# Kernel tuning notes

Measured on AMD Instinct MI355X. Metric: run time of the kernel, lower is better.

Reference implementation:

```python
import jax, jax.numpy as jnp
import numpy as np

B, F, O = 32, 26, 20
IN, G = 2048, 512
REL = 53
EPS = 1e-5  # BatchNorm1d default eps


def setup_inputs() -> dict:
    key = jax.random.key(0)
    ks = jax.random.split(key, 10)
    inp = {
        "region_feats": jax.random.normal(ks[0], (B, F, O, IN), jnp.float32),
        "region_masks": jnp.ones((B, F, O), jnp.float32),
        "rel_feats": jax.random.randint(ks[1], (B, F, O, O), 0, REL, jnp.int64),
        "tem_feats": jax.random.uniform(ks[2], (B, F * O, F * O), jnp.float32),
        # learned params (eval mode: dropout off, BN uses running stats)
        "rel_W": jax.random.normal(ks[3], (G, IN), jnp.float32) * (1.0 / np.sqrt(IN)),
        "rel_b": jnp.zeros((G,), jnp.float32),
        "rel_emb": jax.random.normal(ks[4], (REL, G), jnp.float32) * 0.02,
        "tem_W": jax.random.normal(ks[5], (G, IN), jnp.float32) * (1.0 / np.sqrt(IN)),
        "tem_b": jnp.zeros((G,), jnp.float32),
        "bn_w": jnp.ones((F * O,), jnp.float32),
        "bn_b": jnp.zeros((F * O,), jnp.float32),
        "bn_rm": jnp.zeros((F * O,), jnp.float32),
        "bn_rv": jnp.ones((F * O,), jnp.float32),
    }
    return inp


def reference(region_feats, region_masks, rel_feats, tem_feats,
              rel_W, rel_b, rel_emb, tem_W, tem_b,
              bn_w, bn_b, bn_rm, bn_rv):
    b, f, o, _ = region_feats.shape
    # ---- RELATIONAL FEATURE GRAPH ----
    # [B,F,O,G]
    rel_region = jnp.einsum("bfoi,gi->bfog", region_feats, rel_W) + rel_b
    # embedding lookup: [B,F,O,O,G]
    emb = rel_emb[rel_feats]
    mask = (rel_feats > 0).astype(region_feats.dtype)  # [B,F,O,O]
    msum = jnp.sum(mask, axis=3)                        # [B,F,O]
    # sum_j mask_ij * emb_ij  (masked reduction over neighbor dim)
    emb_sum = jnp.einsum("bfijg,bfij->bfig", emb, mask)
    # sum_j mask_ij * r_i == r_i * msum_i, so (emb_sum + r*msum)/msum
    rel_out = (emb_sum + rel_region * msum[..., None]) / msum[..., None]
    rel_out = rel_out.reshape(b, f * o, -1)
    # ---- TEMPORAL FEATURE GRAPH ----
    tem_region = jnp.einsum("bfoi,gi->bfog", region_feats, tem_W) + tem_b
    tem_region = tem_region.reshape(b, f * o, -1)
    tem_sum = jnp.sum(tem_feats, axis=2)                # [B, F*O]
    tem_out = jnp.matmul(tem_feats, tem_region) / tem_sum[..., None]
    # ---- OUTPUT ----
    out = jnp.concatenate([rel_out, tem_out], axis=-1)  # [B, F*O, 2G]
    out = jnp.tanh(out)
    # BatchNorm1d over channel dim 1 (eval mode, running stats)
    inv = bn_w / jnp.sqrt(bn_rv + EPS)                  # [F*O]
    out = (out - bn_rm[None, :, None]) * inv[None, :, None] + bn_b[None, :, None]
    return out
```

## Files before the change

### kernel.cpp

```cpp
#include <hip/hip_runtime.h>
#include <stdint.h>

#define BB 32
#define FO 520
#define M1 16640
#define KIN 2048
#define KA 2112
#define N1 1024
#define GG 512
#define K2 544
#define M2 640

typedef unsigned short u16;
typedef short v8s __attribute__((ext_vector_type(8)));
typedef float v4f __attribute__((ext_vector_type(4)));

__device__ __forceinline__ u16 f2bf(float f) {
  union { float f; unsigned u; } v; v.f = f;
  unsigned r = v.u + 0x7fffu + ((v.u >> 16) & 1u);
  return (u16)(r >> 16);
}

__device__ __forceinline__ float fast_tanh(float x) {
  float cx = fminf(fmaxf(x, -15.f), 15.f);
  float e = __expf(2.f * cx);
  return (e - 1.f) / (e + 1.f);
}

__global__ void cast8_kernel(const float* __restrict__ rf, const int* __restrict__ rel,
                             u16* __restrict__ A1) {
  const int m = blockIdx.x;
  const int t = threadIdx.x;
  const float4* p = (const float4*)(rf + (size_t)m * KIN);
  u16* orow = A1 + (size_t)m * KA;
  float4 a = p[2 * t], b = p[2 * t + 1];
  v8s v;
  v[0] = (short)f2bf(a.x); v[1] = (short)f2bf(a.y);
  v[2] = (short)f2bf(a.z); v[3] = (short)f2bf(a.w);
  v[4] = (short)f2bf(b.x); v[5] = (short)f2bf(b.y);
  v[6] = (short)f2bf(b.z); v[7] = (short)f2bf(b.w);
  *(v8s*)(orow + t * 8) = v;
  if (t < 64) {
    const int* rp = rel + (size_t)m * 20;
    int cnt = 0, ms = 0;
#pragma unroll
    for (int j = 0; j < 20; ++j) {
      int ix = rp[j];
      cnt += (ix == t + 1);
      ms += (ix > 0);
    }
    float sval = (t < 52 && ms > 0) ? (float)cnt / (float)ms : 0.f;
    orow[KIN + t] = f2bf(sval);
  }
}

__global__ void castw_kernel(const float* __restrict__ relW, const float* __restrict__ temW,
                             const float* __restrict__ emb, u16* __restrict__ o) {
  const int n = blockIdx.x;
  u16* orow = o + (size_t)n * KA;
  const float* src = (n < GG) ? (relW + (size_t)n * KIN) : (temW + (size_t)(n - GG) * KIN);
  for (int k = threadIdx.x; k < KIN; k += 256) orow[k] = f2bf(src[k]);
  for (int k = KIN + threadIdx.x; k < KA; k += 256) {
    int l = k - KIN;
    float v = (n < GG && l < 52) ? emb[(size_t)(l + 1) * GG + n] : 0.f;
    orow[k] = f2bf(v);
  }
}

__global__ void casta2_kernel(const float* __restrict__ tem, u16* __restrict__ A2,
                              float* __restrict__ tsum) {
  const int w = threadIdx.x >> 6;
  const int l = threadIdx.x & 63;
  const int row = blockIdx.x * 4 + w;
  const int b = row / M2, i = row % M2;
  u16* orow = A2 + (size_t)row * K2;
  v8s z = {0, 0, 0, 0, 0, 0, 0, 0};
  if (i >= FO) {
    *(v8s*)(orow + l * 8) = z;
    if (l < 4) *(v8s*)(orow + (64 + l) * 8) = z;
    return;
  }
  const float* srow = tem + ((size_t)b * FO + i) * FO;
  float s = 0.f;
#pragma unroll
  for (int pass = 0; pass < 2; ++pass) {
    int c = (pass == 0) ? l : (64 + l);
    if (pass == 1 && l >= 4) break;
    if (c < 65) {
      float4 a = *(const float4*)(srow + 8 * c);
      float4 bb = *(const float4*)(srow + 8 * c + 4);
      s += a.x + a.y + a.z + a.w + bb.x + bb.y + bb.z + bb.w;
      v8s v;
      v[0] = (short)f2bf(a.x); v[1] = (short)f2bf(a.y);
      v[2] = (short)f2bf(a.z); v[3] = (short)f2bf(a.w);
      v[4] = (short)f2bf(bb.x); v[5] = (short)f2bf(bb.y);
      v[6] = (short)f2bf(bb.z); v[7] = (short)f2bf(bb.w);
      *(v8s*)(orow + c * 8) = v;
    } else {
      *(v8s*)(orow + c * 8) = z;
    }
  }
#pragma unroll
  for (int off = 32; off > 0; off >>= 1) s += __shfl_down(s, off);
  if (l == 0) tsum[(size_t)b * FO + i] = s;
}

__global__ void transp_kernel(const u16* __restrict__ in, u16* __restrict__ o) {
  __shared__ u16 tile[64][66];
  const int jb = blockIdx.x;
  const int gb = blockIdx.y;
  const int b = blockIdx.z;
  const int tx = threadIdx.x, ty = threadIdx.y;
#pragma unroll
  for (int r = 0; r < 8; ++r) {
    int jl = ty + 8 * r;
    int j = jb * 64 + jl;
    unsigned v = 0;
    if (j < FO) v = *(const unsigned*)(in + ((size_t)b * FO + j) * GG + gb * 64 + 2 * tx);
    tile[2 * tx][jl] = (u16)(v & 0xffff);
    tile[2 * tx + 1][jl] = (u16)(v >> 16);
  }
  __syncthreads();
#pragma unroll
  for (int r = 0; r < 8; ++r) {
    int gl = ty + 8 * r;
    int j2 = jb * 64 + 2 * tx;
    if (j2 < K2) {
      unsigned v = *(const unsigned*)&tile[gl][2 * tx];
      *(unsigned*)(o + ((size_t)b * GG + gb * 64 + gl) * K2 + j2) = v;
    }
  }
}

__global__ __launch_bounds__(256) void gemm1_kernel(
    const u16* __restrict__ A, const u16* __restrict__ Wc,
    const float* __restrict__ rel_b, const float* __restrict__ tem_b,
    const float* __restrict__ bn_w, const float* __restrict__ bn_b,
    const float* __restrict__ bn_rm, const float* __restrict__ bn_rv,
    float* __restrict__ out, u16* __restrict__ tem_nat) {
  __shared__ u16 As[128 * 32];
  __shared__ u16 Bs[128 * 32];
  const int tid = threadIdx.x;
  const int lane = tid & 63;
  const int wv = tid >> 6, wm = wv >> 1, wn = wv & 1;
  const int id = blockIdx.x;
  const int x = id & 7, s = id >> 3;
  int mt, ntile;
  if (s < 128) { mt = x * 16 + (s >> 3); ntile = s & 7; }
  else         { mt = 128 + (s - 128);   ntile = x; }
  const int m0 = mt * 128;
  const int n0 = ntile * 128;
  const int quad = lane >> 4, r16 = lane & 15;

  v4f acc[4][4];
#pragma unroll
  for (int i = 0; i < 4; ++i)
#pragma unroll
    for (int j = 0; j < 4; ++j) { v4f z = {0.f, 0.f, 0.f, 0.f}; acc[i][j] = z; }

  for (int k0 = 0; k0 < KA; k0 += 32) {
    __syncthreads();
#pragma unroll
    for (int i = 0; i < 2; ++i) {
      const int L = i * 256 + tid;
      const int r = L >> 2, c = L & 3;
      const u16* ga = A + (size_t)(m0 + r) * KA + k0 + c * 8;
      const u16* gb = Wc + (size_t)(n0 + r) * KA + k0 + c * 8;
      u16* la = &As[(size_t)(i * 256 + wv * 64) * 8];
      u16* lb = &Bs[(size_t)(i * 256 + wv * 64) * 8];
      __builtin_amdgcn_global_load_lds((const __attribute__((address_space(1))) void*)ga,
                                       (__attribute__((address_space(3))) void*)la, 16, 0, 0);
      __builtin_amdgcn_global_load_lds((const __attribute__((address_space(1))) void*)gb,
                                       (__attribute__((address_space(3))) void*)lb, 16, 0, 0);
    }
    __syncthreads();
    v8s af[4], bf[4];
#pragma unroll
    for (int t = 0; t < 4; ++t) {
      af[t] = *(const v8s*)&As[(wm * 64 + t * 16 + r16) * 32 + quad * 8];
      bf[t] = *(const v8s*)&Bs[(wn * 64 + t * 16 + r16) * 32 + quad * 8];
    }
#pragma unroll
    for (int mtt = 0; mtt < 4; ++mtt)
#pragma unroll
      for (int ntt = 0; ntt < 4; ++ntt)
        acc[mtt][ntt] = __builtin_amdgcn_mfma_f32_16x16x32_bf16(af[mtt], bf[ntt], acc[mtt][ntt], 0, 0, 0);
  }

  const bool relhalf = (n0 < GG);
#pragma unroll
  for (int mtt = 0; mtt < 4; ++mtt) {
#pragma unroll
    for (int ntt = 0; ntt < 4; ++ntt) {
      const int n = n0 + wn * 64 + ntt * 16 + r16;
      const int mbase = m0 + wm * 64 + mtt * 16 + quad * 4;
#pragma unroll
      for (int r = 0; r < 4; ++r) {
        const int m = mbase + r;
        float v = acc[mtt][ntt][r];
        if (relhalf) {
          v += rel_b[n];
          const int fo = m % FO;
          float inv = bn_w[fo] * rsqrtf(bn_rv[fo] + 1e-5f);
          out[(size_t)m * N1 + n] = (fast_tanh(v) - bn_rm[fo]) * inv + bn_b[fo];
        } else {
          v += tem_b[n - GG];
          tem_nat[(size_t)m * GG + (n - GG)] = f2bf(v);
        }
      }
    }
  }
}

__global__ __launch_bounds__(256) void gemm2_kernel(
    const u16* __restrict__ A2, const u16* __restrict__ BT,
    const float* __restrict__ tsum,
    const float* __restrict__ bn_w, const float* __restrict__ bn_b,
    const float* __restrict__ bn_rm, const float* __restrict__ bn_rv,
    float* __restrict__ out) {
  __shared__ u16 As[128 * 32];
  __shared__ u16 Bs[128 * 32];
  const int tid = threadIdx.x;
  const int lane = tid & 63;
  const int wv = tid >> 6, wm = wv >> 1, wn = wv & 1;
  const int m0 = blockIdx.x * 128;
  const int n0 = blockIdx.y * 128;
  const int b = blockIdx.z;
  const u16* Ab = A2 + (size_t)b * M2 * K2;
  const u16* Bb = BT + (size_t)b * GG * K2;
  const int quad = lane >> 4, r16 = lane & 15;

  v4f acc[4][4];
#pragma unroll
  for (int i = 0; i < 4; ++i)
#pragma unroll
    for (int j = 0; j < 4; ++j) { v4f z = {0.f, 0.f, 0.f, 0.f}; acc[i][j] = z; }

  for (int k0 = 0; k0 < K2; k0 += 32) {
    __syncthreads();
#pragma unroll
    for (int i = 0; i < 2; ++i) {
      const int L = i * 256 + tid;
      const int r = L >> 2, c = L & 3;
      const u16* ga = Ab + (size_t)(m0 + r) * K2 + k0 + c * 8;
      const u16* gb = Bb + (size_t)(n0 + r) * K2 + k0 + c * 8;
      u16* la = &As[(size_t)(i * 256 + wv * 64) * 8];
      u16* lb = &Bs[(size_t)(i * 256 + wv * 64) * 8];
      __builtin_amdgcn_global_load_lds((const __attribute__((address_space(1))) void*)ga,
                                       (__attribute__((address_space(3))) void*)la, 16, 0, 0);
      __builtin_amdgcn_global_load_lds((const __attribute__((address_space(1))) void*)gb,
                                       (__attribute__((address_space(3))) void*)lb, 16, 0, 0);
    }
    __syncthreads();
    v8s af[4], bf[4];
#pragma unroll
    for (int t = 0; t < 4; ++t) {
      af[t] = *(const v8s*)&As[(wm * 64 + t * 16 + r16) * 32 + quad * 8];
      bf[t] = *(const v8s*)&Bs[(wn * 64 + t * 16 + r16) * 32 + quad * 8];
    }
#pragma unroll
    for (int mt = 0; mt < 4; ++mt)
#pragma unroll
      for (int nt = 0; nt < 4; ++nt)
        acc[mt][nt] = __builtin_amdgcn_mfma_f32_16x16x32_bf16(af[mt], bf[nt], acc[mt][nt], 0, 0, 0);
  }

#pragma unroll
  for (int mt = 0; mt < 4; ++mt) {
#pragma unroll
    for (int nt = 0; nt < 4; ++nt) {
      const int g = n0 + wn * 64 + nt * 16 + r16;
      const int ibase = m0 + wm * 64 + mt * 16 + quad * 4;
#pragma unroll
      for (int r = 0; r < 4; ++r) {
        const int i = ibase + r;
        if (i < FO) {
          float v = acc[mt][nt][r] / tsum[(size_t)b * FO + i];
          float inv = bn_w[i] * rsqrtf(bn_rv[i] + 1e-5f);
          out[((size_t)(b * FO + i)) * N1 + GG + g] =
              (fast_tanh(v) - bn_rm[i]) * inv + bn_b[i];
        }
      }
    }
  }
}

extern "C" void kernel_launch(void* const* d_in, const int* in_sizes, int n_in,
                              void* d_out, int out_size, void* d_ws, size_t ws_size,
                              hipStream_t stream) {
  const float* region_feats = (const float*)d_in[0];
  const int* rel_feats = (const int*)d_in[2];
  const float* tem_feats = (const float*)d_in[3];
  const float* rel_W = (const float*)d_in[4];
  const float* rel_b = (const float*)d_in[5];
  const float* rel_emb = (const float*)d_in[6];
  const float* tem_W = (const float*)d_in[7];
  const float* tem_b = (const float*)d_in[8];
  const float* bn_w = (const float*)d_in[9];
  const float* bn_b = (const float*)d_in[10];
  const float* bn_rm = (const float*)d_in[11];
  const float* bn_rv = (const float*)d_in[12];
  float* out = (float*)d_out;

  char* base = (char*)d_ws;
  u16* A1 = (u16*)base;
  u16* BT = (u16*)base;
  u16* Wc = (u16*)(base + 70287360);
  u16* A2 = (u16*)(base + 74612736);
  u16* tem_nat = (u16*)(base + 96894976);
  float* tsum = (float*)(base + 113934336);

  cast8_kernel<<<16640, 256, 0, stream>>>(region_feats, rel_feats, A1);
  castw_kernel<<<1024, 256, 0, stream>>>(rel_W, tem_W, rel_emb, Wc);
  casta2_kernel<<<5120, 256, 0, stream>>>(tem_feats, A2, tsum);
  gemm1_kernel<<<1040, 256, 0, stream>>>(A1, Wc, rel_b, tem_b,
                                         bn_w, bn_b, bn_rm, bn_rv, out, tem_nat);
  transp_kernel<<<dim3(9, 8, 32), dim3(32, 8), 0, stream>>>(tem_nat, BT);
  gemm2_kernel<<<dim3(5, 4, 32), 256, 0, stream>>>(A2, BT, tsum,
                                                   bn_w, bn_b, bn_rm, bn_rv, out);
}
```

Measured before the change: 461.8 us.

## Fuse weight cast and transpose into neighbours, use BK=64 with XOR-swizzled LDS

Result: faster. 451.5 us (-2.2%).

```diff
diff --git a/kernel.cpp b/kernel.cpp
--- a/kernel.cpp
+++ b/kernel.cpp
@@ -8,7 +8,7 @@
 #define KA 2112
 #define N1 1024
 #define GG 512
-#define K2 544
+#define K2P 576
 #define M2 640
 
 typedef unsigned short u16;
@@ -27,12 +27,23 @@
   return (e - 1.f) / (e + 1.f);
 }
 
-__global__ void cast8_kernel(const float* __restrict__ rf, const int* __restrict__ rel,
-                             u16* __restrict__ A1) {
-  const int m = blockIdx.x;
+__global__ void prep_kernel(const float* __restrict__ rf, const int* __restrict__ rel,
+                            const float* __restrict__ relW, const float* __restrict__ temW,
+                            const float* __restrict__ emb,
+                            u16* __restrict__ A1, u16* __restrict__ Wc) {
+  const int blk = blockIdx.x;
   const int t = threadIdx.x;
-  const float4* p = (const float4*)(rf + (size_t)m * KIN);
-  u16* orow = A1 + (size_t)m * KA;
+  const float* src;
+  u16* orow;
+  if (blk < M1) {
+    src = rf + (size_t)blk * KIN;
+    orow = A1 + (size_t)blk * KA;
+  } else {
+    const int n = blk - M1;
+    src = (n < GG) ? (relW + (size_t)n * KIN) : (temW + (size_t)(n - GG) * KIN);
+    orow = Wc + (size_t)n * KA;
+  }
+  const float4* p = (const float4*)src;
   float4 a = p[2 * t], b = p[2 * t + 1];
   v8s v;
   v[0] = (short)f2bf(a.x); v[1] = (short)f2bf(a.y);
@@ -41,29 +52,22 @@
   v[6] = (short)f2bf(b.z); v[7] = (short)f2bf(b.w);
   *(v8s*)(orow + t * 8) = v;
   if (t < 64) {
-    const int* rp = rel + (size_t)m * 20;
-    int cnt = 0, ms = 0;
-#pragma unroll
-    for (int j = 0; j < 20; ++j) {
-      int ix = rp[j];
-      cnt += (ix == t + 1);
-      ms += (ix > 0);
-    }
-    float sval = (t < 52 && ms > 0) ? (float)cnt / (float)ms : 0.f;
+    float sval = 0.f;
+    if (blk < M1) {
+      const int* rp = rel + (size_t)blk * 20;
+      int cnt = 0, ms = 0;
+#pragma unroll
+      for (int j = 0; j < 20; ++j) {
+        int ix = rp[j];
+        cnt += (ix == t + 1);
+        ms += (ix > 0);
+      }
+      if (t < 52 && ms > 0) sval = (float)cnt / (float)ms;
+    } else {
+      const int n = blk - M1;
+      if (n < GG && t < 52) sval = emb[(size_t)(t + 1) * GG + n];
+    }
     orow[KIN + t] = f2bf(sval);
-  }
-}
-
-__global__ void castw_kernel(const float* __restrict__ relW, const float* __restrict__ temW,
-                             const float* __restrict__ emb, u16* __restrict__ o) {
-  const int n = blockIdx.x;
-  u16* orow = o + (size_t)n * KA;
-  const float* src = (n < GG) ? (relW + (size_t)n * KIN) : (temW + (size_t)(n - GG) * KIN);
-  for (int k = threadIdx.x; k < KIN; k += 256) orow[k] = f2bf(src[k]);
-  for (int k = KIN + threadIdx.x; k < KA; k += 256) {
-    int l = k - KIN;
-    float v = (n < GG && l < 52) ? emb[(size_t)(l + 1) * GG + n] : 0.f;
-    orow[k] = f2bf(v);
   }
 }
 
@@ -73,63 +77,44 @@
   const int l = threadIdx.x & 63;
   const int row = blockIdx.x * 4 + w;
   const int b = row / M2, i = row % M2;
-  u16* orow = A2 + (size_t)row * K2;
+  u16* orow = A2 + (size_t)row * K2P;
   v8s z = {0, 0, 0, 0, 0, 0, 0, 0};
   if (i >= FO) {
     *(v8s*)(orow + l * 8) = z;
-    if (l < 4) *(v8s*)(orow + (64 + l) * 8) = z;
+    if (l < 8) *(v8s*)(orow + (64 + l) * 8) = z;
     return;
   }
   const float* srow = tem + ((size_t)b * FO + i) * FO;
   float s = 0.f;
-#pragma unroll
-  for (int pass = 0; pass < 2; ++pass) {
-    int c = (pass == 0) ? l : (64 + l);
-    if (pass == 1 && l >= 4) break;
-    if (c < 65) {
-      float4 a = *(const float4*)(srow + 8 * c);
-      float4 bb = *(const float4*)(srow + 8 * c + 4);
+  {
+    float4 a = *(const float4*)(srow + 8 * l);
+    float4 bb = *(const float4*)(srow + 8 * l + 4);
+    s += a.x + a.y + a.z + a.w + bb.x + bb.y + bb.z + bb.w;
+    v8s v;
+    v[0] = (short)f2bf(a.x); v[1] = (short)f2bf(a.y);
+    v[2] = (short)f2bf(a.z); v[3] = (short)f2bf(a.w);
+    v[4] = (short)f2bf(bb.x); v[5] = (short)f2bf(bb.y);
+    v[6] = (short)f2bf(bb.z); v[7] = (short)f2bf(bb.w);
+    *(v8s*)(orow + l * 8) = v;
+  }
+  if (l < 8) {
+    if (l == 0) {
+      float4 a = *(const float4*)(srow + 512);
+      float4 bb = *(const float4*)(srow + 516);
       s += a.x + a.y + a.z + a.w + bb.x + bb.y + bb.z + bb.w;
       v8s v;
       v[0] = (short)f2bf(a.x); v[1] = (short)f2bf(a.y);
       v[2] = (short)f2bf(a.z); v[3] = (short)f2bf(a.w);
       v[4] = (short)f2bf(bb.x); v[5] = (short)f2bf(bb.y);
       v[6] = (short)f2bf(bb.z); v[7] = (short)f2bf(bb.w);
-      *(v8s*)(orow + c * 8) = v;
+      *(v8s*)(orow + 512) = v;
     } else {
-      *(v8s*)(orow + c * 8) = z;
+      *(v8s*)(orow + (64 + l) * 8) = z;
     }
   }
 #pragma unroll
   for (int off = 32; off > 0; off >>= 1) s += __shfl_down(s, off);
   if (l == 0) tsum[(size_t)b * FO + i] = s;
-}
-
-__global__ void transp_kernel(const u16* __restrict__ in, u16* __restrict__ o) {
-  __shared__ u16 tile[64][66];
-  const int jb = blockIdx.x;
-  const int gb = blockIdx.y;
-  const int b = blockIdx.z;
-  const int tx = threadIdx.x, ty = threadIdx.y;
-#pragma unroll
-  for (int r = 0; r < 8; ++r) {
-    int jl = ty + 8 * r;
-    int j = jb * 64 + jl;
-    unsigned v = 0;
-    if (j < FO) v = *(const unsigned*)(in + ((size_t)b * FO + j) * GG + gb * 64 + 2 * tx);
-    tile[2 * tx][jl] = (u16)(v & 0xffff);
-    tile[2 * tx + 1][jl] = (u16)(v >> 16);
-  }
-  __syncthreads();
-#pragma unroll
-  for (int r = 0; r < 8; ++r) {
-    int gl = ty + 8 * r;
-    int j2 = jb * 64 + 2 * tx;
-    if (j2 < K2) {
-      unsigned v = *(const unsigned*)&tile[gl][2 * tx];
-      *(unsigned*)(o + ((size_t)b * GG + gb * 64 + gl) * K2 + j2) = v;
-    }
-  }
 }
 
 __global__ __launch_bounds__(256) void gemm1_kernel(
@@ -137,9 +122,10 @@
     const float* __restrict__ rel_b, const float* __restrict__ tem_b,
     const float* __restrict__ bn_w, const float* __restrict__ bn_b,
     const float* __restrict__ bn_rm, const float* __restrict__ bn_rv,
-    float* __restrict__ out, u16* __restrict__ tem_nat) {
-  __shared__ u16 As[128 * 32];
-  __shared__ u16 Bs[128 * 32];
+    float* __restrict__ out, u16* __restrict__ BT) {
+  __shared__ u16 smem[128 * 132];
+  u16* As = smem;
+  u16* Bs = smem + 128 * 64;
   const int tid = threadIdx.x;
   const int lane = tid & 63;
   const int wv = tid >> 6, wm = wv >> 1, wn = wv & 1;
@@ -148,8 +134,7 @@
   int mt, ntile;
   if (s < 128) { mt = x * 16 + (s >> 3); ntile = s & 7; }
   else         { mt = 128 + (s - 128);   ntile = x; }
-  const int m0 = mt * 128;
-  const int n0 = ntile * 128;
+  const int m0 = mt * 128, n0 = ntile * 128;
   const int quad = lane >> 4, r16 = lane & 15;
 
   v4f acc[4][4];
@@ -158,12 +143,13 @@
 #pragma unroll
     for (int j = 0; j < 4; ++j) { v4f z = {0.f, 0.f, 0.f, 0.f}; acc[i][j] = z; }
 
-  for (int k0 = 0; k0 < KA; k0 += 32) {
-    __syncthreads();
-#pragma unroll
-    for (int i = 0; i < 2; ++i) {
+  for (int k0 = 0; k0 < KA; k0 += 64) {
+    __syncthreads();
+#pragma unroll
+    for (int i = 0; i < 4; ++i) {
       const int L = i * 256 + tid;
-      const int r = L >> 2, c = L & 3;
+      const int r = L >> 3;
+      const int c = (L & 7) ^ (r & 7);
       const u16* ga = A + (size_t)(m0 + r) * KA + k0 + c * 8;
       const u16* gb = Wc + (size_t)(n0 + r) * KA + k0 + c * 8;
       u16* la = &As[(size_t)(i * 256 + wv * 64) * 8];
@@ -174,40 +160,75 @@
                                        (__attribute__((address_space(3))) void*)lb, 16, 0, 0);
     }
     __syncthreads();
-    v8s af[4], bf[4];
-#pragma unroll
-    for (int t = 0; t < 4; ++t) {
-      af[t] = *(const v8s*)&As[(wm * 64 + t * 16 + r16) * 32 + quad * 8];
-      bf[t] = *(const v8s*)&Bs[(wn * 64 + t * 16 + r16) * 32 + quad * 8];
-    }
-#pragma unroll
-    for (int mtt = 0; mtt < 4; ++mtt)
-#pragma unroll
-      for (int ntt = 0; ntt < 4; ++ntt)
-        acc[mtt][ntt] = __builtin_amdgcn_mfma_f32_16x16x32_bf16(af[mtt], bf[ntt], acc[mtt][ntt], 0, 0, 0);
-  }
-
-  const bool relhalf = (n0 < GG);
-#pragma unroll
-  for (int mtt = 0; mtt < 4; ++mtt) {
-#pragma unroll
-    for (int ntt = 0; ntt < 4; ++ntt) {
-      const int n = n0 + wn * 64 + ntt * 16 + r16;
-      const int mbase = m0 + wm * 64 + mtt * 16 + quad * 4;
-#pragma unroll
-      for (int r = 0; r < 4; ++r) {
-        const int m = mbase + r;
-        float v = acc[mtt][ntt][r];
-        if (relhalf) {
-          v += rel_b[n];
-          const int fo = m % FO;
-          float inv = bn_w[fo] * rsqrtf(bn_rv[fo] + 1e-5f);
-          out[(size_t)m * N1 + n] = (fast_tanh(v) - bn_rm[fo]) * inv + bn_b[fo];
-        } else {
-          v += tem_b[n - GG];
-          tem_nat[(size_t)m * GG + (n - GG)] = f2bf(v);
+#pragma unroll
+    for (int ks = 0; ks < 2; ++ks) {
+      v8s af[4], bf[4];
+#pragma unroll
+      for (int t4 = 0; t4 < 4; ++t4) {
+        const int ra = wm * 64 + t4 * 16 + r16;
+        const int rb = wn * 64 + t4 * 16 + r16;
+        af[t4] = *(const v8s*)&As[ra * 64 + (((ks * 4 + quad) ^ (ra & 7)) * 8)];
+        bf[t4] = *(const v8s*)&Bs[rb * 64 + (((ks * 4 + quad) ^ (rb & 7)) * 8)];
+      }
+#pragma unroll
+      for (int mtt = 0; mtt < 4; ++mtt)
+#pragma unroll
+        for (int ntt = 0; ntt < 4; ++ntt)
+          acc[mtt][ntt] = __builtin_amdgcn_mfma_f32_16x16x32_bf16(af[mtt], bf[ntt], acc[mtt][ntt], 0, 0, 0);
+    }
+  }
+
+  if (n0 < GG) {
+#pragma unroll
+    for (int mtt = 0; mtt < 4; ++mtt) {
+      const int mb = m0 + wm * 64 + mtt * 16 + quad * 4;
+      const int bb = mb / FO;
+      const int fo0 = mb - bb * FO;
+#pragma unroll
+      for (int ntt = 0; ntt < 4; ++ntt) {
+        const int n = n0 + wn * 64 + ntt * 16 + r16;
+        const float rbn = rel_b[n];
+#pragma unroll
+        for (int r = 0; r < 4; ++r) {
+          const int fo = fo0 + r;
+          const float inv = bn_w[fo] * rsqrtf(bn_rv[fo] + 1e-5f);
+          out[(size_t)(mb + r) * N1 + n] =
+              (fast_tanh(acc[mtt][ntt][r] + rbn) - bn_rm[fo]) * inv + bn_b[fo];
         }
       }
+    }
+  } else {
+    __syncthreads();
+#pragma unroll
+    for (int mtt = 0; mtt < 4; ++mtt) {
+      const int il = wm * 64 + mtt * 16 + quad * 4;
+#pragma unroll
+      for (int ntt = 0; ntt < 4; ++ntt) {
+        const int gl = wn * 64 + ntt * 16 + r16;
+        const float tb = tem_b[(n0 - GG) + gl];
+        ushort4 w;
+        w.x = f2bf(acc[mtt][ntt][0] + tb);
+        w.y = f2bf(acc[mtt][ntt][1] + tb);
+        w.z = f2bf(acc[mtt][ntt][2] + tb);
+        w.w = f2bf(acc[mtt][ntt][3] + tb);
+        *(ushort4*)&smem[gl * 132 + il] = w;
+      }
+    }
+    __syncthreads();
+    const int gl = tid >> 1, seg = tid & 1;
+    const int g = (n0 - GG) + gl;
+    const u16* src = &smem[gl * 132 + seg * 64];
+    const int mbase = m0 + seg * 64;
+#pragma unroll
+    for (int ch = 0; ch < 8; ++ch) {
+      const int m = mbase + ch * 8;
+      const int b1 = m / FO;
+      const int i1 = m - b1 * FO;
+      ushort4 lo = *(const ushort4*)(src + ch * 8);
+      ushort4 hi = *(const ushort4*)(src + ch * 8 + 4);
+      u16* dst = BT + ((size_t)(b1 * GG + g)) * K2P + i1;
+      *(ushort4*)dst = lo;
+      *(ushort4*)(dst + 4) = hi;
     }
   }
 }
@@ -218,16 +239,17 @@
     const float* __restrict__ bn_w, const float* __restrict__ bn_b,
     const float* __restrict__ bn_rm, const float* __restrict__ bn_rv,
     float* __restrict__ out) {
-  __shared__ u16 As[128 * 32];
-  __shared__ u16 Bs[128 * 32];
+  __shared__ u16 smem[2 * 128 * 64];
+  u16* As = smem;
+  u16* Bs = smem + 128 * 64;
   const int tid = threadIdx.x;
   const int lane = tid & 63;
   const int wv = tid >> 6, wm = wv >> 1, wn = wv & 1;
   const int m0 = blockIdx.x * 128;
   const int n0 = blockIdx.y * 128;
   const int b = blockIdx.z;
-  const u16* Ab = A2 + (size_t)b * M2 * K2;
-  const u16* Bb = BT + (size_t)b * GG * K2;
+  const u16* Ab = A2 + (size_t)b * M2 * K2P;
+  const u16* Bb = BT + (size_t)b * GG * K2P;
   const int quad = lane >> 4, r16 = lane & 15;
 
   v4f acc[4][4];
@@ -236,14 +258,15 @@
 #pragma unroll
     for (int j = 0; j < 4; ++j) { v4f z = {0.f, 0.f, 0.f, 0.f}; acc[i][j] = z; }
 
-  for (int k0 = 0; k0 < K2; k0 += 32) {
-    __syncthreads();
-#pragma unroll
-    for (int i = 0; i < 2; ++i) {
+  for (int k0 = 0; k0 < K2P; k0 += 64) {
+    __syncthreads();
+#pragma unroll
+    for (int i = 0; i < 4; ++i) {
       const int L = i * 256 + tid;
-      const int r = L >> 2, c = L & 3;
-      const u16* ga = Ab + (size_t)(m0 + r) * K2 + k0 + c * 8;
-      const u16* gb = Bb + (size_t)(n0 + r) * K2 + k0 + c * 8;
+      const int r = L >> 3;
+      const int c = (L & 7) ^ (r & 7);
+      const u16* ga = Ab + (size_t)(m0 + r) * K2P + k0 + c * 8;
+      const u16* gb = Bb + (size_t)(n0 + r) * K2P + k0 + c * 8;
       u16* la = &As[(size_t)(i * 256 + wv * 64) * 8];
       u16* lb = &Bs[(size_t)(i * 256 + wv * 64) * 8];
       __builtin_amdgcn_global_load_lds((const __attribute__((address_space(1))) void*)ga,
@@ -252,30 +275,35 @@
                                        (__attribute__((address_space(3))) void*)lb, 16, 0, 0);
     }
     __syncthreads();
-    v8s af[4], bf[4];
-#pragma unroll
-    for (int t = 0; t < 4; ++t) {
-      af[t] = *(const v8s*)&As[(wm * 64 + t * 16 + r16) * 32 + quad * 8];
-      bf[t] = *(const v8s*)&Bs[(wn * 64 + t * 16 + r16) * 32 + quad * 8];
-    }
-#pragma unroll
-    for (int mt = 0; mt < 4; ++mt)
-#pragma unroll
-      for (int nt = 0; nt < 4; ++nt)
-        acc[mt][nt] = __builtin_amdgcn_mfma_f32_16x16x32_bf16(af[mt], bf[nt], acc[mt][nt], 0, 0, 0);
-  }
-
-#pragma unroll
-  for (int mt = 0; mt < 4; ++mt) {
-#pragma unroll
-    for (int nt = 0; nt < 4; ++nt) {
-      const int g = n0 + wn * 64 + nt * 16 + r16;
-      const int ibase = m0 + wm * 64 + mt * 16 + quad * 4;
+#pragma unroll
+    for (int ks = 0; ks < 2; ++ks) {
+      v8s af[4], bf[4];
+#pragma unroll
+      for (int t4 = 0; t4 < 4; ++t4) {
+        const int ra = wm * 64 + t4 * 16 + r16;
+        const int rb = wn * 64 + t4 * 16 + r16;
+        af[t4] = *(const v8s*)&As[ra * 64 + (((ks * 4 + quad) ^ (ra & 7)) * 8)];
+        bf[t4] = *(const v8s*)&Bs[rb * 64 + (((ks * 4 + quad) ^ (rb & 7)) * 8)];
+      }
+#pragma unroll
+      for (int mtt = 0; mtt < 4; ++mtt)
+#pragma unroll
+        for (int ntt = 0; ntt < 4; ++ntt)
+          acc[mtt][ntt] = __builtin_amdgcn_mfma_f32_16x16x32_bf16(af[mtt], bf[ntt], acc[mtt][ntt], 0, 0, 0);
+    }
+  }
+
+#pragma unroll
+  for (int mtt = 0; mtt < 4; ++mtt) {
+#pragma unroll
+    for (int ntt = 0; ntt < 4; ++ntt) {
+      const int g = n0 + wn * 64 + ntt * 16 + r16;
+      const int ibase = m0 + wm * 64 + mtt * 16 + quad * 4;
 #pragma unroll
       for (int r = 0; r < 4; ++r) {
         const int i = ibase + r;
         if (i < FO) {
-          float v = acc[mt][nt][r] / tsum[(size_t)b * FO + i];
+          float v = acc[mtt][ntt][r] / tsum[(size_t)b * FO + i];
           float inv = bn_w[i] * rsqrtf(bn_rv[i] + 1e-5f);
           out[((size_t)(b * FO + i)) * N1 + GG + g] =
               (fast_tanh(v) - bn_rm[i]) * inv + bn_b[i];
@@ -304,18 +332,16 @@
 
   char* base = (char*)d_ws;
   u16* A1 = (u16*)base;
-  u16* BT = (u16*)base;
   u16* Wc = (u16*)(base + 70287360);
   u16* A2 = (u16*)(base + 74612736);
-  u16* tem_nat = (u16*)(base + 96894976);
-  float* tsum = (float*)(base + 113934336);
-
-  cast8_kernel<<<16640, 256, 0, stream>>>(region_feats, rel_feats, A1);
-  castw_kernel<<<1024, 256, 0, stream>>>(rel_W, tem_W, rel_emb, Wc);
+  u16* BT = (u16*)(base + 98205696);
+  float* tsum = (float*)(base + 117080064);
+
+  prep_kernel<<<M1 + 1024, 256, 0, stream>>>(region_feats, rel_feats,
+                                             rel_W, tem_W, rel_emb, A1, Wc);
   casta2_kernel<<<5120, 256, 0, stream>>>(tem_feats, A2, tsum);
   gemm1_kernel<<<1040, 256, 0, stream>>>(A1, Wc, rel_b, tem_b,
-                                         bn_w, bn_b, bn_rm, bn_rv, out, tem_nat);
-  transp_kernel<<<dim3(9, 8, 32), dim3(32, 8), 0, stream>>>(tem_nat, BT);
+                                         bn_w, bn_b, bn_rm, bn_rv, out, BT);
   gemm2_kernel<<<dim3(5, 4, 32), 256, 0, stream>>>(A2, BT, tsum,
                                                    bn_w, bn_b, bn_rm, bn_rv, out);
 }
```
